# Kernel optimization log

Measured on AMD Instinct MI355X. Metric: run time of the kernel, lower is better.

## Reference

```python
import jax, jax.numpy as jnp
import numpy as np

S, B, D, H = 1024, 16, 512, 8
DH = D // H  # 64


def setup_inputs() -> dict:
    key = jax.random.key(0)
    k1, k2, k3, k4, k5 = jax.random.split(key, 5)
    x = jax.random.normal(k1, (S, B, D), dtype=jnp.float32)
    # binary validity mask [B, S]: 1 = keep, 0 = masked out (matches torch usage)
    mask = (jax.random.uniform(k2, (B, S)) > 0.2).astype(jnp.float32)
    scale = 1.0 / np.sqrt(D)
    wq = jax.random.normal(k3, (H, DH, D), dtype=jnp.float32) * scale
    wk = jax.random.normal(k4, (H, DH, D), dtype=jnp.float32) * scale
    wv = jax.random.normal(k5, (H, DH, D), dtype=jnp.float32) * scale
    return {"x": x, "mask": mask, "wq": wq, "wk": wk, "wv": wv}


def reference(x, mask, wq, wk, wv):
    # x: [S, B, D]; mask: [B, S]; w*: [H, DH, D] (stacked bias-free Linear weights)
    dh = wq.shape[1]
    # per-hop projections for all hops at once (Linear: y = x @ W.T)
    q = jnp.einsum('sbd,hed->bhse', x, wq)  # [B,H,S,DH]
    k = jnp.einsum('sbd,hed->bhse', x, wk)
    v = jnp.einsum('sbd,hed->bhse', x, wv)
    scores = jnp.einsum('bhse,bhte->bhst', q, k)  # [B,H,S,S]
    inv_mask = (1.0 - mask)[:, None, None, :]      # broadcast over heads, query pos
    align = jnp.tanh(scores / jnp.sqrt(jnp.asarray(dh, x.dtype))) - 10000.0 * inv_mask
    align = jax.nn.softmax(align, axis=-1)
    out = jnp.einsum('bhst,bhte->bhse', align, v)  # [B,H,S,DH]
    s, b = x.shape[0], x.shape[1]
    # concat hops along feature dim, back to seq-first: [S, B, H*DH]
    return jnp.transpose(out, (2, 0, 1, 3)).reshape(s, b, -1)
```

## Files before the change

kernel.cpp:

```cpp
#include <hip/hip_runtime.h>
#include <stdint.h>
#include <stddef.h>

#define SS 1024
#define BB 16
#define DD 512
#define HH 8
#define DHH 64

typedef __attribute__((ext_vector_type(8))) short bf16x8;
typedef __attribute__((ext_vector_type(4))) float f32x4;
typedef __attribute__((ext_vector_type(16))) float f32x16;
typedef __attribute__((ext_vector_type(4))) float float4v;
typedef __attribute__((ext_vector_type(4))) unsigned short us4;

__device__ __forceinline__ unsigned short f2bf(float f) {
  union { float f; unsigned int u; } v; v.f = f;
  unsigned int x = v.u;
  return (unsigned short)((x + 0x7FFFu + ((x >> 16) & 1u)) >> 16);
}

#define GLDS16(dst, src)                                                                  \
  __builtin_amdgcn_global_load_lds(                                                      \
      (const __attribute__((address_space(1))) unsigned int*)(const void*)(src),         \
      (__attribute__((address_space(3))) unsigned int*)(void*)(dst), 16, 0, 0)

__global__ void cvt_kernel(const float* __restrict__ x,
                           const float* __restrict__ wq,
                           const float* __restrict__ wk,
                           const float* __restrict__ wv,
                           const float* __restrict__ mask,
                           unsigned short* __restrict__ xb,
                           unsigned short* __restrict__ wb,
                           float* __restrict__ maskq) {
  const int i = blockIdx.x * 256 + threadIdx.x;
  const int n_x4 = (SS * BB * DD) / 4;
  const int n_w4 = 3 * 65536;
  if (i < n_x4) {
    float4v v = ((const float4v*)x)[i];
    us4 o;
    o[0] = f2bf(v[0]); o[1] = f2bf(v[1]); o[2] = f2bf(v[2]); o[3] = f2bf(v[3]);
    ((us4*)xb)[i] = o;
  } else if (i < n_x4 + n_w4) {
    const int j = i - n_x4;
    const int sel = j >> 16;
    const int off4 = j & 65535;
    const float* wsrc = (sel == 0) ? wq : ((sel == 1) ? wk : wv);
    const float scale = (sel == 0) ? 0.36067376022224085f : 1.0f;
    float4v v = ((const float4v*)wsrc)[off4];
    us4 o;
    o[0] = f2bf(v[0] * scale); o[1] = f2bf(v[1] * scale);
    o[2] = f2bf(v[2] * scale); o[3] = f2bf(v[3] * scale);
    ((us4*)wb)[(sel << 16) + off4] = o;
  } else {
    const int j = i - n_x4 - n_w4;
    float4v mv = ((const float4v*)mask)[j];
    float4v o;
#pragma unroll
    for (int c = 0; c < 4; ++c) o[c] = (mv[c] > 0.5f) ? 0.f : -16384.f;
    ((float4v*)maskq)[j] = o;
  }
}

__global__ __launch_bounds__(256) void proj_kernel(
    const unsigned short* __restrict__ xb,
    const unsigned short* __restrict__ wb,
    unsigned short* __restrict__ qb,
    unsigned short* __restrict__ kb,
    unsigned short* __restrict__ vt) {
  const int bm = blockIdx.x * 128;
  const int bn = blockIdx.y * 128;
  const int b = blockIdx.z / 3;
  const int wsel = blockIdx.z % 3;

  __shared__ unsigned short pool[4 * 64 * 72];
  unsigned short* At = pool;
  unsigned short* Bt = pool + 8192;

  const int tid = threadIdx.x;
  const int w = tid >> 6;
  const int lane = tid & 63;

  const unsigned short* wptr = wb + wsel * (512 * DD);

  f32x4 acc[4][4];
#pragma unroll
  for (int mi = 0; mi < 4; ++mi)
#pragma unroll
    for (int ni = 0; ni < 4; ++ni) acc[mi][ni] = (f32x4){0.f, 0.f, 0.f, 0.f};

  const int m0 = (w & 1) * 64;
  const int n0 = (w >> 1) * 64;

  for (int kt = 0; kt < 8; ++kt) {
#pragma unroll
    for (int i = 0; i < 4; ++i) {
      const int c = i * 256 + tid;
      const int r = c >> 3;
      const int c8 = (c & 7) ^ (r & 7);
      GLDS16(&At[(i * 256 + w * 64) * 8],
             xb + (size_t)(bm + r) * (BB * DD) + b * DD + kt * 64 + c8 * 8);
      GLDS16(&Bt[(i * 256 + w * 64) * 8],
             wptr + (size_t)(bn + r) * DD + kt * 64 + c8 * 8);
    }
    __syncthreads();
#pragma unroll
    for (int ks = 0; ks < 2; ++ks) {
      const int sw = ((ks * 4 + (lane >> 4)) ^ (lane & 7)) << 4;
      bf16x8 af[4], bfr[4];
#pragma unroll
      for (int mi = 0; mi < 4; ++mi)
        af[mi] = *(const bf16x8*)((const char*)At + (m0 + mi * 16 + (lane & 15)) * 128 + sw);
#pragma unroll
      for (int ni = 0; ni < 4; ++ni)
        bfr[ni] = *(const bf16x8*)((const char*)Bt + (n0 + ni * 16 + (lane & 15)) * 128 + sw);
#pragma unroll
      for (int mi = 0; mi < 4; ++mi)
#pragma unroll
        for (int ni = 0; ni < 4; ++ni)
          acc[mi][ni] =
              __builtin_amdgcn_mfma_f32_16x16x32_bf16(af[mi], bfr[ni], acc[mi][ni], 0, 0, 0);
    }
    __syncthreads();
  }

  const int h = (bn + n0) >> 6;
  unsigned short* OTw = pool + w * 4608;
  if (wsel != 2) {
#pragma unroll
    for (int mi = 0; mi < 4; ++mi)
#pragma unroll
      for (int ni = 0; ni < 4; ++ni)
#pragma unroll
        for (int j = 0; j < 4; ++j)
          OTw[(mi * 16 + (lane >> 4) * 4 + j) * 72 + ni * 16 + (lane & 15)] =
              f2bf(acc[mi][ni][j]);
  } else {
#pragma unroll
    for (int mi = 0; mi < 4; ++mi)
#pragma unroll
      for (int ni = 0; ni < 4; ++ni) {
        us4 pk;
#pragma unroll
        for (int j = 0; j < 4; ++j) pk[j] = f2bf(acc[mi][ni][j]);
        *(us4*)&OTw[(ni * 16 + (lane & 15)) * 72 + mi * 16 + (lane >> 4) * 4] = pk;
      }
  }
  unsigned short* gout = (wsel == 0) ? qb : ((wsel == 1) ? kb : vt);
#pragma unroll
  for (int pass = 0; pass < 8; ++pass) {
    const int row = pass * 8 + (lane >> 3);
    bf16x8 vrow = *(const bf16x8*)&OTw[row * 72 + (lane & 7) * 8];
    size_t dst;
    if (wsel != 2)
      dst = ((size_t)(b * HH + h) * SS + (size_t)(bm + m0 + row)) * DHH + (lane & 7) * 8;
    else
      dst = ((size_t)(b * HH + h) * DHH + (size_t)row) * SS + (bm + m0) + (lane & 7) * 8;
    *(bf16x8*)&gout[dst] = vrow;
  }
}

__global__ __launch_bounds__(256, 4) void attn_kernel(
    const unsigned short* __restrict__ qb,
    const unsigned short* __restrict__ kb,
    const unsigned short* __restrict__ vt,
    const float* __restrict__ maskq,
    float* __restrict__ out) {
  const int id = blockIdx.x;
  const int xcd = id & 7;
  const int slot = id >> 3;
  const int bh = xcd * 16 + (slot >> 3);
  const int qt = slot & 7;
  const int b = bh >> 3;
  const int h = bh & 7;
  const int tid = threadIdx.x;
  const int w = tid >> 6;
  const int lane = tid & 63;
  const int l31 = lane & 31;
  const int hi32 = lane >> 5;
  const int sl = (l31 & 0x13) | ((l31 & 4) << 1) | ((l31 & 8) >> 1);

  __shared__ unsigned short Ks[2][64 * 64];
  __shared__ unsigned short Vs[2][64 * 64];
  __shared__ float rs_s[4][32];

  const size_t base_qk = (size_t)bh * SS * DHH;
  const int q0 = qt * 128 + w * 32;

  bf16x8 aq[4];
  {
    const unsigned short* qp = qb + base_qk + (size_t)(q0 + l31) * DHH + hi32 * 8;
    aq[0] = *(const bf16x8*)(qp);
    aq[1] = *(const bf16x8*)(qp + 16);
    aq[2] = *(const bf16x8*)(qp + 32);
    aq[3] = *(const bf16x8*)(qp + 48);
  }

  const int sr0 = w * 16 + (lane >> 3);
  const int sxb = (((lane & 7) ^ (lane >> 3)) << 4);
  const unsigned short* ksrc0 = kb + base_qk + (size_t)sr0 * DHH + (sxb >> 1);
  const unsigned short* ksrc1 = ksrc0 + 8 * DHH;
  const unsigned short* vsrc0 =
      vt + (size_t)bh * DHH * SS + (size_t)sr0 * SS + (sxb >> 1);
  const unsigned short* vsrc1 = vsrc0 + 8 * SS;

#define STAGE(bb, kt2)                                                       \
  do {                                                                       \
    GLDS16(&Ks[bb][(w * 16) * 64], ksrc0 + (size_t)(kt2) * (64 * DHH));      \
    GLDS16(&Ks[bb][(w * 16 + 8) * 64], ksrc1 + (size_t)(kt2) * (64 * DHH));  \
    GLDS16(&Vs[bb][(w * 16) * 64], vsrc0 + (size_t)(kt2) * 64);              \
    GLDS16(&Vs[bb][(w * 16 + 8) * 64], vsrc1 + (size_t)(kt2) * 64);          \
  } while (0)

  STAGE(0, 0);

  f32x16 accO[2];
#pragma unroll
  for (int n = 0; n < 2; ++n)
#pragma unroll
    for (int i = 0; i < 16; ++i) accO[n][i] = 0.f;
  float rs = 0.f;
  const float* mrow = maskq + b * SS;

  __syncthreads();

  int buf = 0;
  for (int kt = 0; kt < 16; ++kt) {
    if (kt < 15) STAGE(buf ^ 1, kt + 1);
    const char* Kb = (const char*)&Ks[buf][0];
    const char* Vb = (const char*)&Vs[buf][0];

    const int ksw = (sl & 7) << 4;
    f32x16 scT[2];
    scT[0] = (f32x16){};
    scT[1] = (f32x16){};
    __builtin_amdgcn_s_setprio(1);
#pragma unroll
    for (int ks = 0; ks < 4; ++ks) {
      bf16x8 kfA = *(const bf16x8*)(Kb + (0 + sl) * 128 + ((ks * 32 + hi32 * 16) ^ ksw));
      scT[0] = __builtin_amdgcn_mfma_f32_32x32x16_bf16(kfA, aq[ks], scT[0], 0, 0, 0);
    }
#pragma unroll
    for (int ks = 0; ks < 4; ++ks) {
      bf16x8 kfB = *(const bf16x8*)(Kb + (32 + sl) * 128 + ((ks * 32 + hi32 * 16) ^ ksw));
      scT[1] = __builtin_amdgcn_mfma_f32_32x32x16_bf16(kfB, aq[ks], scT[1], 0, 0, 0);
    }
    __builtin_amdgcn_s_setprio(0);

#pragma unroll
    for (int T = 0; T < 2; ++T) {
      const f32x16 sc = scT[T];
      unsigned int pu[16];
#pragma unroll
      for (int g = 0; g < 4; ++g) {
        float4v mv = *(const float4v*)&mrow[kt * 64 + T * 32 + (g >> 1) * 16 +
                                            hi32 * 8 + (g & 1) * 4];
        float a0 = 1.f + __builtin_amdgcn_exp2f(sc[g * 4 + 0]);
        float a1 = 1.f + __builtin_amdgcn_exp2f(sc[g * 4 + 1]);
        float a2 = 1.f + __builtin_amdgcn_exp2f(sc[g * 4 + 2]);
        float a3 = 1.f + __builtin_amdgcn_exp2f(sc[g * 4 + 3]);
        float p01 = a0 * a1, p23 = a2 * a3;
        float rq = __builtin_amdgcn_rcpf(p01 * p23);
        float r01 = p23 * rq, r23 = p01 * rq;
        float r[4];
        r[0] = a1 * r01; r[1] = a0 * r01; r[2] = a3 * r23; r[3] = a2 * r23;
#pragma unroll
        for (int i = 0; i < 4; ++i) {
          float p = __builtin_amdgcn_exp2f(__builtin_fmaf(r[i], -2.88539008178f, mv[i]));
          rs += p;
          union { float f; unsigned int u; } cv;
          cv.f = p;
          pu[g * 4 + i] = cv.u;
        }
      }
      union { unsigned int u[4]; bf16x8 v; } f0, f1;
#pragma unroll
      for (int m = 0; m < 4; ++m) {
        f0.u[m] = __builtin_amdgcn_perm(pu[2 * m + 1], pu[2 * m], 0x07060302u);
        f1.u[m] = __builtin_amdgcn_perm(pu[8 + 2 * m + 1], pu[8 + 2 * m], 0x07060302u);
      }
      __builtin_amdgcn_s_setprio(1);
#pragma unroll
      for (int n = 0; n < 2; ++n) {
        const int vrow = n * 32 + l31;
        const int vsw = (vrow & 7) << 4;
        bf16x8 bv0 = *(const bf16x8*)(Vb + vrow * 128 + (((T * 2 + 0) * 32 + hi32 * 16) ^ vsw));
        bf16x8 bv1 = *(const bf16x8*)(Vb + vrow * 128 + (((T * 2 + 1) * 32 + hi32 * 16) ^ vsw));
        accO[n] = __builtin_amdgcn_mfma_f32_32x32x16_bf16(f0.v, bv0, accO[n], 0, 0, 0);
        accO[n] = __builtin_amdgcn_mfma_f32_32x32x16_bf16(f1.v, bv1, accO[n], 0, 0, 0);
      }
      __builtin_amdgcn_s_setprio(0);
    }
    __syncthreads();
    buf ^= 1;
  }
#undef STAGE

  rs += __shfl_xor(rs, 32, 64);
  if (hi32 == 0) rs_s[w][l31] = __builtin_amdgcn_rcpf(rs);
  float4v ri[4];
#pragma unroll
  for (int g = 0; g < 4; ++g) ri[g] = *(const float4v*)&rs_s[w][g * 8 + hi32 * 4];

#pragma unroll
  for (int n = 0; n < 2; ++n)
#pragma unroll
    for (int g = 0; g < 4; ++g)
#pragma unroll
      for (int i = 0; i < 4; ++i) {
        const int qrow = q0 + g * 8 + hi32 * 4 + i;
        out[((size_t)qrow * BB + b) * DD + h * DHH + n * 32 + l31] =
            accO[n][g * 4 + i] * ri[g][i];
      }
}

extern "C" void kernel_launch(void* const* d_in, const int* in_sizes, int n_in,
                              void* d_out, int out_size, void* d_ws, size_t ws_size,
                              hipStream_t stream) {
  const float* x = (const float*)d_in[0];
  const float* mask = (const float*)d_in[1];
  const float* wq = (const float*)d_in[2];
  const float* wk = (const float*)d_in[3];
  const float* wv = (const float*)d_in[4];
  float* out = (float*)d_out;

  char* ws = (char*)d_ws;
  unsigned short* xb = (unsigned short*)(ws);
  unsigned short* wb = (unsigned short*)(ws + (16ull << 20));
  float* maskq = (float*)(ws + (17ull << 20) + (512ull << 10));
  unsigned short* qb = (unsigned short*)(ws + (18ull << 20));
  unsigned short* kb = (unsigned short*)(ws + (34ull << 20));
  unsigned short* vt = (unsigned short*)(ws + (50ull << 20));

  cvt_kernel<<<dim3(8976), 256, 0, stream>>>(x, wq, wk, wv, mask, xb, wb, maskq);
  proj_kernel<<<dim3(8, 4, 48), 256, 0, stream>>>(xb, wb, qb, kb, vt);
  attn_kernel<<<dim3(1024), 256, 0, stream>>>(qb, kb, vt, maskq, out);
}
```

Baseline: 115.1 us.

## Compute softmax row sums via MFMA with ones and remap proj grid per XCD

The attention kernel now accumulates each row's softmax denominator with two extra MFMAs that multiply the bf16 probabilities by a ones vector. This replaces per-element scalar adds, the cross-lane shuffle and the shared-memory broadcast of reciprocals. The row sums now come from bf16-rounded probabilities, which matches the values actually used in the PV product. The projection kernel moves to a 1D grid whose block index is remapped so that blocks sharing the same batch and weight select land on the same XCD, aiming at better L2 reuse.

```diff
diff --git a/kernel.cpp b/kernel.cpp
--- a/kernel.cpp
+++ b/kernel.cpp
@@ -68,10 +68,15 @@
     unsigned short* __restrict__ qb,
     unsigned short* __restrict__ kb,
     unsigned short* __restrict__ vt) {
-  const int bm = blockIdx.x * 128;
-  const int bn = blockIdx.y * 128;
-  const int b = blockIdx.z / 3;
-  const int wsel = blockIdx.z % 3;
+  const int id = blockIdx.x;
+  const int xcd = id & 7;
+  const int j = id >> 3;
+  const int z = (j >> 5) * 8 + xcd;
+  const int xy = j & 31;
+  const int bm = (xy & 7) * 128;
+  const int bn = (xy >> 3) * 128;
+  const int b = z / 3;
+  const int wsel = z % 3;
 
   __shared__ unsigned short pool[4 * 64 * 72];
   unsigned short* At = pool;
@@ -132,9 +137,9 @@
 #pragma unroll
       for (int ni = 0; ni < 4; ++ni)
 #pragma unroll
-        for (int j = 0; j < 4; ++j)
-          OTw[(mi * 16 + (lane >> 4) * 4 + j) * 72 + ni * 16 + (lane & 15)] =
-              f2bf(acc[mi][ni][j]);
+        for (int jj = 0; jj < 4; ++jj)
+          OTw[(mi * 16 + (lane >> 4) * 4 + jj) * 72 + ni * 16 + (lane & 15)] =
+              f2bf(acc[mi][ni][jj]);
   } else {
 #pragma unroll
     for (int mi = 0; mi < 4; ++mi)
@@ -142,7 +147,7 @@
       for (int ni = 0; ni < 4; ++ni) {
         us4 pk;
 #pragma unroll
-        for (int j = 0; j < 4; ++j) pk[j] = f2bf(acc[mi][ni][j]);
+        for (int jj = 0; jj < 4; ++jj) pk[jj] = f2bf(acc[mi][ni][jj]);
         *(us4*)&OTw[(ni * 16 + (lane & 15)) * 72 + mi * 16 + (lane >> 4) * 4] = pk;
       }
   }
@@ -182,7 +187,6 @@
 
   __shared__ unsigned short Ks[2][64 * 64];
   __shared__ unsigned short Vs[2][64 * 64];
-  __shared__ float rs_s[4][32];
 
   const size_t base_qk = (size_t)bh * SS * DHH;
   const int q0 = qt * 128 + w * 32;
@@ -196,6 +200,11 @@
     aq[3] = *(const bf16x8*)(qp + 48);
   }
 
+  union { unsigned short u[8]; bf16x8 v; } ones_;
+#pragma unroll
+  for (int i = 0; i < 8; ++i) ones_.u[i] = 0x3F80;
+  const bf16x8 ones = ones_.v;
+
   const int sr0 = w * 16 + (lane >> 3);
   const int sxb = (((lane & 7) ^ (lane >> 3)) << 4);
   const unsigned short* ksrc0 = kb + base_qk + (size_t)sr0 * DHH + (sxb >> 1);
@@ -219,7 +228,7 @@
   for (int n = 0; n < 2; ++n)
 #pragma unroll
     for (int i = 0; i < 16; ++i) accO[n][i] = 0.f;
-  float rs = 0.f;
+  f32x16 rsacc = {};
   const float* mrow = maskq + b * SS;
 
   __syncthreads();
@@ -267,7 +276,6 @@
 #pragma unroll
         for (int i = 0; i < 4; ++i) {
           float p = __builtin_amdgcn_exp2f(__builtin_fmaf(r[i], -2.88539008178f, mv[i]));
-          rs += p;
           union { float f; unsigned int u; } cv;
           cv.f = p;
           pu[g * 4 + i] = cv.u;
@@ -280,6 +288,8 @@
         f1.u[m] = __builtin_amdgcn_perm(pu[8 + 2 * m + 1], pu[8 + 2 * m], 0x07060302u);
       }
       __builtin_amdgcn_s_setprio(1);
+      rsacc = __builtin_amdgcn_mfma_f32_32x32x16_bf16(f0.v, ones, rsacc, 0, 0, 0);
+      rsacc = __builtin_amdgcn_mfma_f32_32x32x16_bf16(f1.v, ones, rsacc, 0, 0, 0);
 #pragma unroll
       for (int n = 0; n < 2; ++n) {
         const int vrow = n * 32 + l31;
@@ -296,22 +306,17 @@
   }
 #undef STAGE
 
-  rs += __shfl_xor(rs, 32, 64);
-  if (hi32 == 0) rs_s[w][l31] = __builtin_amdgcn_rcpf(rs);
-  float4v ri[4];
-#pragma unroll
-  for (int g = 0; g < 4; ++g) ri[g] = *(const float4v*)&rs_s[w][g * 8 + hi32 * 4];
-
-#pragma unroll
-  for (int n = 0; n < 2; ++n)
-#pragma unroll
-    for (int g = 0; g < 4; ++g)
-#pragma unroll
-      for (int i = 0; i < 4; ++i) {
-        const int qrow = q0 + g * 8 + hi32 * 4 + i;
-        out[((size_t)qrow * BB + b) * DD + h * DHH + n * 32 + l31] =
-            accO[n][g * 4 + i] * ri[g][i];
-      }
+#pragma unroll
+  for (int g = 0; g < 4; ++g)
+#pragma unroll
+    for (int i = 0; i < 4; ++i) {
+      const int r = g * 4 + i;
+      const float rinv = __builtin_amdgcn_rcpf(rsacc[r]);
+      const int qrow = q0 + g * 8 + hi32 * 4 + i;
+#pragma unroll
+      for (int n = 0; n < 2; ++n)
+        out[((size_t)qrow * BB + b) * DD + h * DHH + n * 32 + l31] = accO[n][r] * rinv;
+    }
 }
 
 extern "C" void kernel_launch(void* const* d_in, const int* in_sizes, int n_in,
@@ -333,6 +338,6 @@
   unsigned short* vt = (unsigned short*)(ws + (50ull << 20));
 
   cvt_kernel<<<dim3(8976), 256, 0, stream>>>(x, wq, wk, wv, mask, xb, wb, maskq);
-  proj_kernel<<<dim3(8, 4, 48), 256, 0, stream>>>(xb, wb, qb, kb, vt);
+  proj_kernel<<<dim3(1536), 256, 0, stream>>>(xb, wb, qb, kb, vt);
   attn_kernel<<<dim3(1024), 256, 0, stream>>>(qb, kb, vt, maskq, out);
 }
```

Result: slower. 120.5 us (+4.8%).
